# Optimization experiments

Measured on AMD Instinct MI355X. Metric: run time of the kernel, lower is better.

## Reference

```python
import jax, jax.numpy as jnp
import numpy as np

QUALITY = 50.0
TEMP = 0.3  # soft-round temperature

_LUM = np.array([[16,11,10,16,24,40,51,61],[12,12,14,19,26,58,60,55],[14,13,16,24,40,57,69,56],[14,17,22,29,51,87,80,62],[18,22,37,56,68,109,103,77],[24,35,55,64,81,104,113,92],[49,64,78,87,103,121,120,101],[72,92,95,98,112,100,103,99]], dtype=np.float32)
_CHR = np.array([[17,18,24,47,99,99,99,99],[18,21,26,66,99,99,99,99],[24,26,56,99,99,99,99,99],[47,66,99,99,99,99,99,99],[99,99,99,99,99,99,99,99],[99,99,99,99,99,99,99,99],[99,99,99,99,99,99,99,99],[99,99,99,99,99,99,99,99]], dtype=np.float32)

def _scaled_qtable(base, qf):
    qf = max(1.0, min(100.0, qf))
    s = 5000.0 / qf if qf < 50 else 200.0 - 2.0 * qf
    return np.maximum(np.floor((base * s + 50.0) / 100.0), 1.0)

# Per-channel quantization tables: Y uses luminance, Cb/Cr use chrominance. (3,8,8)
QTAB = jnp.asarray(np.stack([_scaled_qtable(_LUM, QUALITY), _scaled_qtable(_CHR, QUALITY), _scaled_qtable(_CHR, QUALITY)]).astype(np.float32))

# The original 64x1x8x8 conv kernel factors as outer product D[u,x]*D[v,y].
_u = np.arange(8)[:, None]
_x = np.arange(8)[None, :]
_c = np.where(_u == 0, 1.0 / np.sqrt(2.0), 1.0)
DCT = jnp.asarray((0.5 * _c * np.cos((2 * _x + 1) * _u * np.pi / 16.0)).astype(np.float32))

M_FWD = jnp.array([[0.299, 0.587, 0.114], [-0.168736, -0.331264, 0.5], [0.5, -0.418688, -0.081312]], dtype=jnp.float32)
M_INV = jnp.array([[1.0, 0.0, 1.402], [1.0, -0.344136, -0.714136], [1.0, 1.772, 0.0]], dtype=jnp.float32)
OFF = jnp.array([0.0, 0.5, 0.5], dtype=jnp.float32)


def setup_inputs() -> dict:
    key = jax.random.key(0)
    x = jax.random.uniform(key, (32, 3, 512, 512), dtype=jnp.float32)
    return {"x": x}


def reference(x):
    B, C, H, W = x.shape  # H, W divisible by 8 (no pad branch)
    # RGB -> YCbCr, centered
    ycbcr = jnp.einsum('ij,bjhw->bihw', M_FWD, x) + OFF[None, :, None, None] - 0.5
    # split into 8x8 blocks: (B, 3, H/8, 8, W/8, 8)
    blocks = ycbcr.reshape(B, C, H // 8, 8, W // 8, 8)
    # block DCT: coef[u,v] = sum_{x,y} D[u,x] D[v,y] block[x,y]
    coef = jnp.einsum('ux,vy,bchxgy->bchugv', DCT, DCT, blocks)
    q = QTAB[None, :, None, :, None, :]  # broadcast per-channel table
    d = coef / q
    # smooth rounding: x + 0.5*tanh(50*T*(x - round(x)))
    sr = d + 0.5 * jnp.tanh(50.0 * TEMP * (d - jnp.round(d)))
    deq = sr * q
    # block IDCT (transpose of DCT): block[x,y] = sum_{u,v} D[u,x] D[v,y] coef[u,v]
    rec = jnp.einsum('ux,vy,bchugv->bchxgy', DCT, DCT, deq)
    ycbcr_rec = rec.reshape(B, C, H, W) + 0.5
    rgb = jnp.einsum('ij,bjhw->bihw', M_INV, ycbcr_rec - OFF[None, :, None, None])
    return jnp.clip(rgb, 0.0, 1.0)
```

## Files before the change

kernel.cpp:

```cpp
#include <hip/hip_runtime.h>
#include <math.h>

#define A0c 0.35355339059327373f
#define C1c 0.4903926402016152f
#define C2c 0.46193976625564337f
#define C3c 0.41573480615127262f
#define C5c 0.27778511650980114f
#define C6c 0.19134171618254492f
#define C7c 0.09754516100806417f

#define IMG_W 512
#define IMG_HW (512 * 512)

typedef float f8v __attribute__((ext_vector_type(8)));

__device__ const float QLUMT[64] = {
    16,12,14,14,18,24,49,72,
    11,12,13,17,22,35,64,92,
    10,14,16,22,37,55,78,95,
    16,19,24,29,56,64,87,98,
    24,26,40,51,68,81,103,112,
    40,58,57,87,109,104,121,100,
    51,60,69,80,103,113,120,103,
    61,55,56,62,77,92,101,99};
__device__ const float QCHRT[64] = {
    17,18,24,47,99,99,99,99,
    18,21,26,66,99,99,99,99,
    24,26,56,99,99,99,99,99,
    47,66,99,99,99,99,99,99,
    99,99,99,99,99,99,99,99,
    99,99,99,99,99,99,99,99,
    99,99,99,99,99,99,99,99,
    99,99,99,99,99,99,99,99};

__device__ __forceinline__ void fdct8(float v[8]) {
    float s0 = v[0] + v[7], s1 = v[1] + v[6], s2 = v[2] + v[5], s3 = v[3] + v[4];
    float d0 = v[0] - v[7], d1 = v[1] - v[6], d2 = v[2] - v[5], d3 = v[3] - v[4];
    float e0 = s0 + s3, e1 = s1 + s2, f0 = s0 - s3, f1 = s1 - s2;
    v[0] = A0c * (e0 + e1);
    v[4] = A0c * (e0 - e1);
    v[2] = C2c * f0 + C6c * f1;
    v[6] = C6c * f0 - C2c * f1;
    v[1] = C1c * d0 + C3c * d1 + C5c * d2 + C7c * d3;
    v[3] = C3c * d0 - C7c * d1 - C1c * d2 - C5c * d3;
    v[5] = C5c * d0 - C1c * d1 + C7c * d2 + C3c * d3;
    v[7] = C7c * d0 - C5c * d1 + C3c * d2 - C1c * d3;
}

__device__ __forceinline__ void idct8(float v[8]) {
    float g0 = v[0], g1 = v[1], g2 = v[2], g3 = v[3];
    float g4 = v[4], g5 = v[5], g6 = v[6], g7 = v[7];
    float ep = A0c * (g0 + g4), em = A0c * (g0 - g4);
    float t26a = C2c * g2 + C6c * g6;
    float t26b = C6c * g2 - C2c * g6;
    float e0 = ep + t26a, e1 = em + t26b, e2 = em - t26b, e3 = ep - t26a;
    float o0 = C1c * g1 + C3c * g3 + C5c * g5 + C7c * g7;
    float o1 = C3c * g1 - C7c * g3 - C1c * g5 - C5c * g7;
    float o2 = C5c * g1 - C1c * g3 + C7c * g5 + C3c * g7;
    float o3 = C7c * g1 - C5c * g3 + C3c * g5 - C1c * g7;
    v[0] = e0 + o0; v[7] = e0 - o0;
    v[1] = e1 + o1; v[6] = e1 - o1;
    v[2] = e2 + o2; v[5] = e2 - o2;
    v[3] = e3 + o3; v[4] = e3 - o3;
}

#define K_EXP2 43.2808512266689f
__device__ __forceinline__ float softq(float x, float q, float rq) {
    float d = x * rq;
    float rn = rintf(d);
    float t = d - rn;
    float e2 = __builtin_amdgcn_exp2f(K_EXP2 * t);
    float th = (e2 - 1.0f) * __builtin_amdgcn_rcpf(e2 + 1.0f);
    return (d + 0.5f * th) * q;
}

template <int CTRL>
__device__ __forceinline__ float fdpp(float x) {
    return __int_as_float(__builtin_amdgcn_mov_dpp(__float_as_int(x), CTRL, 0xF, 0xF, false));
}
__device__ __forceinline__ float fswz4(float x) {
    return __int_as_float(__builtin_amdgcn_ds_swizzle(__float_as_int(x), 0x101F));
}

__device__ __forceinline__ void xpose8(float v[8], bool rb0, bool rb1, bool rb2) {
    float t[8];
#pragma unroll
    for (int i = 0; i < 8; ++i) t[i] = fdpp<0xB1>(v[i ^ 1]);
#pragma unroll
    for (int i = 0; i < 8; ++i) v[i] = (((i & 1) != 0) == rb0) ? v[i] : t[i];
#pragma unroll
    for (int i = 0; i < 8; ++i) t[i] = fdpp<0x4E>(v[i ^ 2]);
#pragma unroll
    for (int i = 0; i < 8; ++i) v[i] = (((i & 2) != 0) == rb1) ? v[i] : t[i];
#pragma unroll
    for (int i = 0; i < 8; ++i) t[i] = fswz4(v[i ^ 4]);
#pragma unroll
    for (int i = 0; i < 8; ++i) v[i] = (((i & 4) != 0) == rb2) ? v[i] : t[i];
}

__global__ __launch_bounds__(256) void jpeg_kernel(const float* __restrict__ x,
                                                   float* __restrict__ out) {
    const int tid = threadIdx.x;
    const int wid = tid >> 6;
    const int lane = tid & 63;

    const int gw = blockIdx.x * 4 + wid;
    const int bimg = gw >> 9;
    const int rem = gw & 511;
    const int gh = rem >> 3;
    const int tx = rem & 7;

    const int r = lane & 7;
    const int blk = lane >> 3;

    const bool rb0 = (r & 1) != 0, rb1 = (r & 2) != 0, rb2 = (r & 4) != 0;

    const size_t off = (size_t)bimg * 3 * IMG_HW +
                       (size_t)(gh * 8 + r) * IMG_W + tx * 64 + blk * 8;
    const float* base = x + off;

    const f8v Rv = *(const f8v*)(base);
    const f8v Gv = *(const f8v*)(base + IMG_HW);
    const f8v Bv = *(const f8v*)(base + 2 * IMG_HW);

    const f8v qL = *(const f8v*)&QLUMT[r * 8];
    const f8v qC = *(const f8v*)&QCHRT[r * 8];
    f8v rqL, rqC;
#pragma unroll
    for (int u = 0; u < 8; ++u) {
        rqL[u] = __builtin_amdgcn_rcpf(qL[u]);
        rqC[u] = __builtin_amdgcn_rcpf(qC[u]);
    }

    float g0[8], g1[8], g2[8];
#pragma unroll
    for (int k = 0; k < 8; ++k) {
        float R = Rv[k], G = Gv[k], B = Bv[k];
        g0[k] = 0.299f * R + 0.587f * G + 0.114f * B - 0.5f;
        g1[k] = -0.168736f * R - 0.331264f * G + 0.5f * B;
        g2[k] = 0.5f * R - 0.418688f * G - 0.081312f * B;
    }

    fdct8(g0);
    xpose8(g0, rb0, rb1, rb2);
    fdct8(g0);
#pragma unroll
    for (int u = 0; u < 8; ++u) g0[u] = softq(g0[u], qL[u], rqL[u]);
    idct8(g0);
    xpose8(g0, rb0, rb1, rb2);
    idct8(g0);

    fdct8(g1);
    xpose8(g1, rb0, rb1, rb2);
    fdct8(g1);
#pragma unroll
    for (int u = 0; u < 8; ++u) g1[u] = softq(g1[u], qC[u], rqC[u]);
    idct8(g1);
    xpose8(g1, rb0, rb1, rb2);
    idct8(g1);

    fdct8(g2);
    xpose8(g2, rb0, rb1, rb2);
    fdct8(g2);
#pragma unroll
    for (int u = 0; u < 8; ++u) g2[u] = softq(g2[u], qC[u], rqC[u]);
    idct8(g2);
    xpose8(g2, rb0, rb1, rb2);
    idct8(g2);

    f8v Ro, Go, Bo;
#pragma unroll
    for (int k = 0; k < 8; ++k) {
        float Y  = g0[k] + 0.5f;
        float Cb = g1[k];
        float Cr = g2[k];
        float R = Y + 1.402f * Cr;
        float G = Y - 0.344136f * Cb - 0.714136f * Cr;
        float B = Y + 1.772f * Cb;
        Ro[k] = fminf(fmaxf(R, 0.0f), 1.0f);
        Go[k] = fminf(fmaxf(G, 0.0f), 1.0f);
        Bo[k] = fminf(fmaxf(B, 0.0f), 1.0f);
    }
    float* obase = out + off;
    *(f8v*)(obase) = Ro;
    *(f8v*)(obase + IMG_HW) = Go;
    *(f8v*)(obase + 2 * IMG_HW) = Bo;
}

extern "C" void kernel_launch(void* const* d_in, const int* in_sizes, int n_in,
                              void* d_out, int out_size, void* d_ws, size_t ws_size,
                              hipStream_t stream) {
    const float* x = (const float*)d_in[0];
    float* out = (float*)d_out;
    const int B = in_sizes[0] / (3 * IMG_HW);
    const int n_wg = B * 128;
    hipLaunchKernelGGL(jpeg_kernel, dim3(n_wg), dim3(256), 0, stream, x, out);
}
```

Before: 46.35 us.

## Pack DCT math into float2 ops, transpose via LDS, use nontemporal stores

Rewrites the DCT/IDCT, color conversion and soft-quantization as 2-wide float vector ops so the compiler can emit packed FP32 instructions. It replaces the DPP/swizzle register transpose with a padded per-wave LDS transpose and swaps the thread-to-row mapping so global loads change coalescing pattern. The softq dequant is simplified algebraically to x + (q/2)*tanh, and output stores become nontemporal. It adds LDS traffic and relies on the wave-synchronous LDS exchange without barriers; the kernel is likely memory-bound, so compute savings may matter little.

```diff
diff --git a/kernel.cpp b/kernel.cpp
--- a/kernel.cpp
+++ b/kernel.cpp
@@ -1,5 +1,11 @@
 #include <hip/hip_runtime.h>
 #include <math.h>
+
+#define IMG_W 512
+#define IMG_HW (512 * 512)
+
+typedef float f8v __attribute__((ext_vector_type(8)));
+typedef float f2v __attribute__((ext_vector_type(2)));
 
 #define A0c 0.35355339059327373f
 #define C1c 0.4903926402016152f
@@ -8,11 +14,6 @@
 #define C5c 0.27778511650980114f
 #define C6c 0.19134171618254492f
 #define C7c 0.09754516100806417f
-
-#define IMG_W 512
-#define IMG_HW (512 * 512)
-
-typedef float f8v __attribute__((ext_vector_type(8)));
 
 __device__ const float QLUMT[64] = {
     16,12,14,14,18,24,49,72,
@@ -33,73 +34,66 @@
     99,99,99,99,99,99,99,99,
     99,99,99,99,99,99,99,99};
 
+__device__ __forceinline__ f2v mk2(float a, float b) { f2v r; r[0] = a; r[1] = b; return r; }
+
 __device__ __forceinline__ void fdct8(float v[8]) {
-    float s0 = v[0] + v[7], s1 = v[1] + v[6], s2 = v[2] + v[5], s3 = v[3] + v[4];
-    float d0 = v[0] - v[7], d1 = v[1] - v[6], d2 = v[2] - v[5], d3 = v[3] - v[4];
-    float e0 = s0 + s3, e1 = s1 + s2, f0 = s0 - s3, f1 = s1 - s2;
-    v[0] = A0c * (e0 + e1);
-    v[4] = A0c * (e0 - e1);
-    v[2] = C2c * f0 + C6c * f1;
-    v[6] = C6c * f0 - C2c * f1;
-    v[1] = C1c * d0 + C3c * d1 + C5c * d2 + C7c * d3;
-    v[3] = C3c * d0 - C7c * d1 - C1c * d2 - C5c * d3;
-    v[5] = C5c * d0 - C1c * d1 + C7c * d2 + C3c * d3;
-    v[7] = C7c * d0 - C5c * d1 + C3c * d2 - C1c * d3;
+    f2v a01 = mk2(v[0], v[1]), b01 = mk2(v[7], v[6]);
+    f2v a23 = mk2(v[2], v[3]), b23 = mk2(v[5], v[4]);
+    f2v S01 = a01 + b01;
+    f2v S23 = a23 + b23;
+    f2v D01 = a01 - b01;
+    f2v D23 = a23 - b23;
+    f2v E = S01 + mk2(S23[1], S23[0]);
+    f2v F = S01 - mk2(S23[1], S23[0]);
+    f2v V04 = A0c * (mk2(E[0], E[0]) + mk2(E[1], -E[1]));
+    v[0] = V04[0]; v[4] = V04[1];
+    f2v V26 = mk2(C2c, C6c) * mk2(F[0], F[0]) + mk2(C6c, -C2c) * mk2(F[1], F[1]);
+    v[2] = V26[0]; v[6] = V26[1];
+    f2v d0b = mk2(D01[0], D01[0]), d1b = mk2(D01[1], D01[1]);
+    f2v d2b = mk2(D23[0], D23[0]), d3b = mk2(D23[1], D23[1]);
+    f2v V13 = mk2(C1c, C3c) * d0b + mk2(C3c, -C7c) * d1b
+            + mk2(C5c, -C1c) * d2b + mk2(C7c, -C5c) * d3b;
+    v[1] = V13[0]; v[3] = V13[1];
+    f2v V57 = mk2(C5c, C7c) * d0b + mk2(-C1c, -C5c) * d1b
+            + mk2(C7c, C3c) * d2b + mk2(C3c, -C1c) * d3b;
+    v[5] = V57[0]; v[7] = V57[1];
 }
 
 __device__ __forceinline__ void idct8(float v[8]) {
     float g0 = v[0], g1 = v[1], g2 = v[2], g3 = v[3];
     float g4 = v[4], g5 = v[5], g6 = v[6], g7 = v[7];
-    float ep = A0c * (g0 + g4), em = A0c * (g0 - g4);
-    float t26a = C2c * g2 + C6c * g6;
-    float t26b = C6c * g2 - C2c * g6;
-    float e0 = ep + t26a, e1 = em + t26b, e2 = em - t26b, e3 = ep - t26a;
-    float o0 = C1c * g1 + C3c * g3 + C5c * g5 + C7c * g7;
-    float o1 = C3c * g1 - C7c * g3 - C1c * g5 - C5c * g7;
-    float o2 = C5c * g1 - C1c * g3 + C7c * g5 + C3c * g7;
-    float o3 = C7c * g1 - C5c * g3 + C3c * g5 - C1c * g7;
-    v[0] = e0 + o0; v[7] = e0 - o0;
-    v[1] = e1 + o1; v[6] = e1 - o1;
-    v[2] = e2 + o2; v[5] = e2 - o2;
-    v[3] = e3 + o3; v[4] = e3 - o3;
+    f2v EPM = A0c * (mk2(g0, g0) + mk2(g4, -g4));
+    f2v T26 = mk2(C2c, C6c) * mk2(g2, g2) + mk2(C6c, -C2c) * mk2(g6, g6);
+    f2v E01 = EPM + T26;
+    f2v E23 = mk2(EPM[1], EPM[0]) - mk2(T26[1], T26[0]);
+    f2v g1b = mk2(g1, g1), g3b = mk2(g3, g3), g5b = mk2(g5, g5), g7b = mk2(g7, g7);
+    f2v O01 = mk2(C1c, C3c) * g1b + mk2(C3c, -C7c) * g3b
+            + mk2(C5c, -C1c) * g5b + mk2(C7c, -C5c) * g7b;
+    f2v O23 = mk2(C5c, C7c) * g1b + mk2(-C1c, -C5c) * g3b
+            + mk2(C7c, C3c) * g5b + mk2(C3c, -C1c) * g7b;
+    f2v R01 = E01 + O01; f2v R76 = E01 - O01;
+    f2v R23 = E23 + O23; f2v R54 = E23 - O23;
+    v[0] = R01[0]; v[1] = R01[1]; v[7] = R76[0]; v[6] = R76[1];
+    v[2] = R23[0]; v[3] = R23[1]; v[5] = R54[0]; v[4] = R54[1];
 }
 
 #define K_EXP2 43.2808512266689f
-__device__ __forceinline__ float softq(float x, float q, float rq) {
-    float d = x * rq;
-    float rn = rintf(d);
-    float t = d - rn;
-    float e2 = __builtin_amdgcn_exp2f(K_EXP2 * t);
-    float th = (e2 - 1.0f) * __builtin_amdgcn_rcpf(e2 + 1.0f);
-    return (d + 0.5f * th) * q;
-}
-
-template <int CTRL>
-__device__ __forceinline__ float fdpp(float x) {
-    return __int_as_float(__builtin_amdgcn_mov_dpp(__float_as_int(x), CTRL, 0xF, 0xF, false));
-}
-__device__ __forceinline__ float fswz4(float x) {
-    return __int_as_float(__builtin_amdgcn_ds_swizzle(__float_as_int(x), 0x101F));
-}
-
-__device__ __forceinline__ void xpose8(float v[8], bool rb0, bool rb1, bool rb2) {
-    float t[8];
-#pragma unroll
-    for (int i = 0; i < 8; ++i) t[i] = fdpp<0xB1>(v[i ^ 1]);
-#pragma unroll
-    for (int i = 0; i < 8; ++i) v[i] = (((i & 1) != 0) == rb0) ? v[i] : t[i];
-#pragma unroll
-    for (int i = 0; i < 8; ++i) t[i] = fdpp<0x4E>(v[i ^ 2]);
-#pragma unroll
-    for (int i = 0; i < 8; ++i) v[i] = (((i & 2) != 0) == rb1) ? v[i] : t[i];
-#pragma unroll
-    for (int i = 0; i < 8; ++i) t[i] = fswz4(v[i ^ 4]);
-#pragma unroll
-    for (int i = 0; i < 8; ++i) v[i] = (((i & 4) != 0) == rb2) ? v[i] : t[i];
+__device__ __forceinline__ f2v softq2(f2v x, f2v qh, f2v rq) {
+    f2v d = x * rq;
+    f2v t = d - mk2(rintf(d[0]), rintf(d[1]));
+    float ea = __builtin_amdgcn_exp2f(K_EXP2 * t[0]);
+    float eb = __builtin_amdgcn_exp2f(K_EXP2 * t[1]);
+    f2v e2 = mk2(ea, eb);
+    f2v num = e2 - 1.0f;
+    f2v th = num * mk2(__builtin_amdgcn_rcpf(e2[0] + 1.0f),
+                       __builtin_amdgcn_rcpf(e2[1] + 1.0f));
+    return x + qh * th;
 }
 
 __global__ __launch_bounds__(256) void jpeg_kernel(const float* __restrict__ x,
                                                    float* __restrict__ out) {
+    __shared__ float xpose[4][768];
+
     const int tid = threadIdx.x;
     const int wid = tid >> 6;
     const int lane = tid & 63;
@@ -110,10 +104,8 @@
     const int gh = rem >> 3;
     const int tx = rem & 7;
 
-    const int r = lane & 7;
-    const int blk = lane >> 3;
-
-    const bool rb0 = (r & 1) != 0, rb1 = (r & 2) != 0, rb2 = (r & 4) != 0;
+    const int r = lane >> 3;
+    const int blk = lane & 7;
 
     const size_t off = (size_t)bimg * 3 * IMG_HW +
                        (size_t)(gh * 8 + r) * IMG_W + tx * 64 + blk * 8;
@@ -123,68 +115,87 @@
     const f8v Gv = *(const f8v*)(base + IMG_HW);
     const f8v Bv = *(const f8v*)(base + 2 * IMG_HW);
 
-    const f8v qL = *(const f8v*)&QLUMT[r * 8];
-    const f8v qC = *(const f8v*)&QCHRT[r * 8];
-    f8v rqL, rqC;
+    const f8v qLf = *(const f8v*)&QLUMT[r * 8];
+    const f8v qCf = *(const f8v*)&QCHRT[r * 8];
+    f8v qhL, rqL, qhC, rqC;
 #pragma unroll
     for (int u = 0; u < 8; ++u) {
-        rqL[u] = __builtin_amdgcn_rcpf(qL[u]);
-        rqC[u] = __builtin_amdgcn_rcpf(qC[u]);
-    }
+        qhL[u] = 0.5f * qLf[u];  rqL[u] = __builtin_amdgcn_rcpf(qLf[u]);
+        qhC[u] = 0.5f * qCf[u];  rqC[u] = __builtin_amdgcn_rcpf(qCf[u]);
+    }
+
+    float* xp = xpose[wid];
+    const int wbase = blk * 12 + r;
+    const int rbase = r * 96 + blk * 12;
 
     float g0[8], g1[8], g2[8];
 #pragma unroll
-    for (int k = 0; k < 8; ++k) {
-        float R = Rv[k], G = Gv[k], B = Bv[k];
-        g0[k] = 0.299f * R + 0.587f * G + 0.114f * B - 0.5f;
-        g1[k] = -0.168736f * R - 0.331264f * G + 0.5f * B;
-        g2[k] = 0.5f * R - 0.418688f * G - 0.081312f * B;
-    }
-
-    fdct8(g0);
-    xpose8(g0, rb0, rb1, rb2);
-    fdct8(g0);
-#pragma unroll
-    for (int u = 0; u < 8; ++u) g0[u] = softq(g0[u], qL[u], rqL[u]);
-    idct8(g0);
-    xpose8(g0, rb0, rb1, rb2);
-    idct8(g0);
-
-    fdct8(g1);
-    xpose8(g1, rb0, rb1, rb2);
-    fdct8(g1);
-#pragma unroll
-    for (int u = 0; u < 8; ++u) g1[u] = softq(g1[u], qC[u], rqC[u]);
-    idct8(g1);
-    xpose8(g1, rb0, rb1, rb2);
-    idct8(g1);
-
-    fdct8(g2);
-    xpose8(g2, rb0, rb1, rb2);
-    fdct8(g2);
-#pragma unroll
-    for (int u = 0; u < 8; ++u) g2[u] = softq(g2[u], qC[u], rqC[u]);
-    idct8(g2);
-    xpose8(g2, rb0, rb1, rb2);
-    idct8(g2);
+    for (int k = 0; k < 8; k += 2) {
+        f2v R = mk2(Rv[k], Rv[k + 1]);
+        f2v G = mk2(Gv[k], Gv[k + 1]);
+        f2v B = mk2(Bv[k], Bv[k + 1]);
+        f2v Y  = 0.299f * R + 0.587f * G + 0.114f * B - 0.5f;
+        f2v Cb = -0.168736f * R - 0.331264f * G + 0.5f * B;
+        f2v Cr = 0.5f * R - 0.418688f * G - 0.081312f * B;
+        g0[k] = Y[0];  g0[k + 1] = Y[1];
+        g1[k] = Cb[0]; g1[k + 1] = Cb[1];
+        g2[k] = Cr[0]; g2[k + 1] = Cr[1];
+    }
+
+#pragma unroll
+    for (int ch = 0; ch < 3; ++ch) {
+        float* g = (ch == 0) ? g0 : (ch == 1) ? g1 : g2;
+        const f8v qh = (ch == 0) ? qhL : qhC;
+        const f8v rq = (ch == 0) ? rqL : rqC;
+
+        fdct8(g);
+#pragma unroll
+        for (int v = 0; v < 8; ++v) xp[v * 96 + wbase] = g[v];
+        {
+            float4 lo = *(const float4*)&xp[rbase];
+            float4 hi = *(const float4*)&xp[rbase + 4];
+            g[0] = lo.x; g[1] = lo.y; g[2] = lo.z; g[3] = lo.w;
+            g[4] = hi.x; g[5] = hi.y; g[6] = hi.z; g[7] = hi.w;
+        }
+        fdct8(g);
+#pragma unroll
+        for (int u = 0; u < 8; u += 2) {
+            f2v s = softq2(mk2(g[u], g[u + 1]), mk2(qh[u], qh[u + 1]), mk2(rq[u], rq[u + 1]));
+            g[u] = s[0]; g[u + 1] = s[1];
+        }
+        idct8(g);
+#pragma unroll
+        for (int xr = 0; xr < 8; ++xr) xp[xr * 96 + wbase] = g[xr];
+        {
+            float4 lo = *(const float4*)&xp[rbase];
+            float4 hi = *(const float4*)&xp[rbase + 4];
+            g[0] = lo.x; g[1] = lo.y; g[2] = lo.z; g[3] = lo.w;
+            g[4] = hi.x; g[5] = hi.y; g[6] = hi.z; g[7] = hi.w;
+        }
+        idct8(g);
+    }
 
     f8v Ro, Go, Bo;
 #pragma unroll
-    for (int k = 0; k < 8; ++k) {
-        float Y  = g0[k] + 0.5f;
-        float Cb = g1[k];
-        float Cr = g2[k];
-        float R = Y + 1.402f * Cr;
-        float G = Y - 0.344136f * Cb - 0.714136f * Cr;
-        float B = Y + 1.772f * Cb;
-        Ro[k] = fminf(fmaxf(R, 0.0f), 1.0f);
-        Go[k] = fminf(fmaxf(G, 0.0f), 1.0f);
-        Bo[k] = fminf(fmaxf(B, 0.0f), 1.0f);
+    for (int k = 0; k < 8; k += 2) {
+        f2v Y  = mk2(g0[k], g0[k + 1]) + 0.5f;
+        f2v Cb = mk2(g1[k], g1[k + 1]);
+        f2v Cr = mk2(g2[k], g2[k + 1]);
+        f2v R = Y + 1.402f * Cr;
+        f2v G = Y - 0.344136f * Cb - 0.714136f * Cr;
+        f2v B = Y + 1.772f * Cb;
+        f2v zero = mk2(0.0f, 0.0f), one = mk2(1.0f, 1.0f);
+        R = __builtin_elementwise_min(__builtin_elementwise_max(R, zero), one);
+        G = __builtin_elementwise_min(__builtin_elementwise_max(G, zero), one);
+        B = __builtin_elementwise_min(__builtin_elementwise_max(B, zero), one);
+        Ro[k] = R[0]; Ro[k + 1] = R[1];
+        Go[k] = G[0]; Go[k + 1] = G[1];
+        Bo[k] = B[0]; Bo[k + 1] = B[1];
     }
     float* obase = out + off;
-    *(f8v*)(obase) = Ro;
-    *(f8v*)(obase + IMG_HW) = Go;
-    *(f8v*)(obase + 2 * IMG_HW) = Bo;
+    __builtin_nontemporal_store(Ro, (f8v*)(obase));
+    __builtin_nontemporal_store(Go, (f8v*)(obase + IMG_HW));
+    __builtin_nontemporal_store(Bo, (f8v*)(obase + 2 * IMG_HW));
 }
 
 extern "C" void kernel_launch(void* const* d_in, const int* in_sizes, int n_in,
```

Measured after the change: 56.09 us. +21.0%, slower.
